# Kernel tuning notes

Hardware: AMD Instinct MI355X
Metric: run time of the kernel (lower is better)

Reference implementation:

```python
import jax, jax.numpy as jnp
import numpy as np

N = 50000
E = 800000
P = 400000
D_IN = 128
D_HID = 128


def setup_inputs() -> dict:
    key = jax.random.key(0)
    k = jax.random.split(key, 7)
    edge_index = jax.random.randint(k[0], (2, E), 0, N, dtype=jnp.int32)
    edge_pairs = jax.random.randint(k[1], (2, P), 0, N, dtype=jnp.int32)
    emb = jax.random.normal(k[2], (N, D_IN), dtype=jnp.float32)
    W1 = jax.random.normal(k[3], (D_IN, D_HID), dtype=jnp.float32) * (1.0 / np.sqrt(D_IN))
    b1 = jnp.zeros((D_HID,), dtype=jnp.float32)
    W2 = jax.random.normal(k[4], (D_HID, D_HID), dtype=jnp.float32) * (1.0 / np.sqrt(D_HID))
    b2 = jnp.zeros((D_HID,), dtype=jnp.float32)
    return {"edge_index": edge_index, "edge_pairs": edge_pairs, "emb": emb,
            "W1": W1, "b1": b1, "W2": W2, "b2": b2}


def gcn_conv(x, W, b, src, dst):
    """PyG GCNConv: add self-loops, symmetric deg^-1/2 normalization,
    linear transform, scatter-add aggregation into destination nodes."""
    n = x.shape[0]
    loop = jnp.arange(n, dtype=src.dtype)
    s = jnp.concatenate([src, loop])  # [E+N]
    d = jnp.concatenate([dst, loop])
    deg = jax.ops.segment_sum(jnp.ones_like(d, dtype=x.dtype), d, num_segments=n)
    dinv = jnp.where(deg > 0, jax.lax.rsqrt(jnp.maximum(deg, 1e-12)), 0.0)
    norm = dinv[s] * dinv[d]  # [E+N]
    h = x @ W  # [N, out]
    msg = h[s] * norm[:, None]  # gather + scale
    out = jax.ops.segment_sum(msg, d, num_segments=n)  # scatter-add
    return out + b


def reference(edge_index, edge_pairs, emb, W1, b1, W2, b2):
    src, dst = edge_index[0], edge_index[1]
    # encode (eval mode: dropout is identity)
    z = jax.nn.relu(gcn_conv(emb, W1, b1, src, dst))
    z = gcn_conv(z, W2, b2, src, dst)
    # decode: dot product per candidate pair
    return jnp.sum(z[edge_pairs[0]] * z[edge_pairs[1]], axis=1)  # [P]
```

## Files before the change

kernel.cpp:

```cpp
#include <hip/hip_runtime.h>


typedef __attribute__((ext_vector_type(8))) short short8;
typedef __attribute__((ext_vector_type(4))) float floatx4;

#define STAGE_G 128

__device__ __forceinline__ unsigned short f2bf(float f) {
    union { float f; unsigned int u; } v; v.f = f;
    unsigned int u = v.u;
    u += 0x7fffu + ((u >> 16) & 1u);
    return (unsigned short)(u >> 16);
}

__device__ __forceinline__ unsigned int pack2(float a, float b) {
    return (unsigned int)f2bf(a) | ((unsigned int)f2bf(b) << 16);
}

__device__ __forceinline__ float4 cvt4(uint2 u) {
    float4 f;
    f.x = __uint_as_float(u.x << 16);
    f.y = __uint_as_float(u.x & 0xffff0000u);
    f.z = __uint_as_float(u.y << 16);
    f.w = __uint_as_float(u.y & 0xffff0000u);
    return f;
}


__global__ __launch_bounds__(256) void block_hist_kernel(const int* __restrict__ dst,
                                                         int* __restrict__ bhist,
                                                         int E, int NB) {
    __shared__ int bh[1024];
    int t = threadIdx.x, g = blockIdx.x;
    for (int b = t; b < NB; b += 256) bh[b] = 0;
    __syncthreads();
    int chunk = (E + gridDim.x - 1) / gridDim.x;
    int lo = g * chunk, hi = min(lo + chunk, E);
    for (int i = lo + t; i < hi; i += 256) atomicAdd(&bh[dst[i] >> 6], 1);
    __syncthreads();
    for (int b = t; b < NB; b += 256) bhist[g * NB + b] = bh[b];
}

__global__ __launch_bounds__(128) void s1_scan_blocks(int* __restrict__ bhist,
                                                      int* __restrict__ T, int NB) {
    __shared__ int s[2][128];
    int b = blockIdx.x, t = threadIdx.x;
    int v = bhist[t * NB + b];
    int cur = 0;
    s[0][t] = v;
    __syncthreads();
#pragma unroll
    for (int off = 1; off < 128; off <<= 1) {
        int nxt = cur ^ 1;
        int val = s[cur][t];
        if (t >= off) val += s[cur][t - off];
        s[nxt][t] = val;
        __syncthreads();
        cur = nxt;
    }
    int inc = s[cur][t];
    bhist[t * NB + b] = inc - v;
    if (t == 127) T[b] = inc;
}

__global__ __launch_bounds__(256) void s2_scan_buckets(const int* __restrict__ T,
                                                       int* __restrict__ bucket_base, int NB) {
    __shared__ int sums[256];
    int t = threadIdx.x;
    int chunk = (NB + 255) >> 8;
    int lo = t * chunk, hi = min(lo + chunk, NB);
    int s = 0;
    for (int i = lo; i < hi; ++i) s += T[i];
    sums[t] = s;
    __syncthreads();
    if (t == 0) {
        int run = 0;
        for (int i = 0; i < 256; ++i) { int v = sums[i]; sums[i] = run; run += v; }
    }
    __syncthreads();
    int run = sums[t];
    for (int i = lo; i < hi; ++i) { bucket_base[i] = run; run += T[i]; }
    if (lo < NB && hi == NB) bucket_base[NB] = run;
}

__global__ __launch_bounds__(256) void stage_kernel(const int* __restrict__ src,
                                                    const int* __restrict__ dst,
                                                    const int* __restrict__ bhist,
                                                    const int* __restrict__ bucket_base,
                                                    unsigned int* __restrict__ stage,
                                                    int E, int NB) {
    __shared__ int lcur[1024];
    int t = threadIdx.x, g = blockIdx.x;
    for (int b = t; b < NB; b += 256) lcur[b] = bucket_base[b] + bhist[g * NB + b];
    __syncthreads();
    int chunk = (E + gridDim.x - 1) / gridDim.x;
    int lo = g * chunk, hi = min(lo + chunk, E);
    for (int i = lo + t; i < hi; i += 256) {
        int d = dst[i];
        int pos = atomicAdd(&lcur[d >> 6], 1);
        stage[pos] = ((unsigned int)src[i] << 6) | (unsigned int)(d & 63);
    }
}

__global__ __launch_bounds__(256) void scatter_kernel(const unsigned int* __restrict__ stage,
                                                      const int* __restrict__ bucket_base,
                                                      int* __restrict__ row_ptr,
                                                      float* __restrict__ dinv,
                                                      int* __restrict__ srcs_sorted,
                                                      int N) {
    __shared__ int cnt[64];
    __shared__ int lcur[64];
    int b = blockIdx.x, t = threadIdx.x;
    int lo = b << 6;
    int base = bucket_base[b], basen = bucket_base[b + 1];
    if (t < 64) cnt[t] = 0;
    __syncthreads();
    for (int i = base + t; i < basen; i += 256) atomicAdd(&cnt[stage[i] & 63u], 1);
    __syncthreads();
    if (t < 64) {
        int v = cnt[t];
        int inc = v;
#pragma unroll
        for (int off = 1; off < 64; off <<= 1) {
            int x = __shfl_up(inc, off, 64);
            if (t >= off) inc += x;
        }
        int exc = inc - v;
        int node = lo + t;
        if (node < N) {
            row_ptr[node] = base + exc;
            dinv[node] = rsqrtf((float)(v + 1));
            if (node == N - 1) row_ptr[N] = base + exc + v;
        }
        lcur[t] = base + exc;
    }
    __syncthreads();
    for (int i = base + t; i < basen; i += 256) {
        unsigned int rec = stage[i];
        int pos = atomicAdd(&lcur[rec & 63u], 1);
        srcs_sorted[pos] = (int)(rec >> 6);
    }
}

template <bool BF16IN>
__global__ __launch_bounds__(256) void gemm_mfma_kernel(const void* __restrict__ Xv,
                                                        const float* __restrict__ W,
                                                        const float* __restrict__ dinv,
                                                        uint2* __restrict__ H, int N) {
    __shared__ __align__(16) char smem[50176];
    short* WB = (short*)smem;
    short* XL = (short*)(smem + 32768);
    float* Cst = (float*)smem;

    const int tid = threadIdx.x;
    const int w = tid >> 6;
    const int lane = tid & 63;
    const int blk = blockIdx.x;

    {
        const float4* W4 = (const float4*)W;
#pragma unroll
        for (int i = 0; i < 16; ++i) {
            int f = tid + i * 256;
            int k = f >> 5;
            int c4 = f & 31;
            float4 wv = W4[f];
            int kt = k >> 5, q = (k >> 3) & 3, j = k & 7;
            float e[4] = {wv.x, wv.y, wv.z, wv.w};
#pragma unroll
            for (int m = 0; m < 4; ++m) {
                int c = c4 * 4 + m;
                int nt = c >> 4;
                int ln = q * 16 + (c & 15);
                WB[((nt * 4 + kt) * 64 + ln) * 8 + j] = (short)f2bf(e[m]);
            }
        }
    }
    {
#pragma unroll
        for (int i = 0; i < 8; ++i) {
            int f = tid + i * 256;
            int row = f >> 5;
            int c4 = f & 31;
            int gr = min(blk * 64 + row, N - 1);
            uint2 u;
            if constexpr (BF16IN) {
                u = ((const uint2*)Xv)[(size_t)gr * 32 + c4];
            } else {
                float4 xv = ((const float4*)Xv)[(size_t)gr * 32 + c4];
                u.x = pack2(xv.x, xv.y);
                u.y = pack2(xv.z, xv.w);
            }
            *(uint2*)&XL[row * 136 + c4 * 4] = u;
        }
    }
    __syncthreads();

    const int arow = w * 16 + (lane & 15);
    const int koff = (lane >> 4) * 8;
    short8 a[4];
#pragma unroll
    for (int kt = 0; kt < 4; ++kt)
        a[kt] = *(const short8*)&XL[arow * 136 + kt * 32 + koff];

    floatx4 acc[8];
#pragma unroll
    for (int nt = 0; nt < 8; ++nt) acc[nt] = (floatx4){0.f, 0.f, 0.f, 0.f};

#pragma unroll
    for (int kt = 0; kt < 4; ++kt) {
#pragma unroll
        for (int nt = 0; nt < 8; ++nt) {
            short8 b = *(const short8*)&WB[((nt * 4 + kt) * 64 + lane) * 8];
            acc[nt] = __builtin_amdgcn_mfma_f32_16x16x32_bf16(a[kt], b, acc[nt], 0, 0, 0);
        }
    }
    __syncthreads();

    {
        int q = lane >> 4, cn = lane & 15;
#pragma unroll
        for (int nt = 0; nt < 8; ++nt)
#pragma unroll
            for (int r = 0; r < 4; ++r)
                Cst[(w * 16 + q * 4 + r) * 132 + nt * 16 + cn] = acc[nt][r];
    }
    __syncthreads();
    {
#pragma unroll
        for (int i = 0; i < 8; ++i) {
            int f = tid + i * 256;
            int row = f >> 5;
            int c4 = f & 31;
            int gr = blk * 64 + row;
            if (gr < N) {
                float4 v = *(float4*)&Cst[row * 132 + c4 * 4];
                float di = dinv[gr];
                uint2 o;
                o.x = pack2(v.x * di, v.y * di);
                o.y = pack2(v.z * di, v.w * di);
                H[(size_t)gr * 32 + c4] = o;
            }
        }
    }
}

__global__ __launch_bounds__(256) void agg_kernel(const unsigned short* __restrict__ Hp,
                                                  const int* __restrict__ row_ptr,
                                                  const int* __restrict__ srcs,
                                                  const float* __restrict__ dinv,
                                                  const float* __restrict__ bias,
                                                  unsigned short* __restrict__ Z,
                                                  int N, int do_relu) {
    int gw = (int)((blockIdx.x * blockDim.x + threadIdx.x) >> 6);
    int lane = threadIdx.x & 63;
    int half = lane >> 5;
    int hl = lane & 31;
    int n = gw * 2 + half;
    if (n >= N) return;

    const uint2* H2 = (const uint2*)Hp;
    float4 a0 = cvt4(H2[(size_t)n * 32 + hl]);
    float4 a1 = make_float4(0.f, 0.f, 0.f, 0.f);
    float4 a2 = make_float4(0.f, 0.f, 0.f, 0.f);
    float4 a3 = make_float4(0.f, 0.f, 0.f, 0.f);

    int j = row_ptr[n], end = row_ptr[n + 1];
    for (; j + 7 < end; j += 8) {
        uint2 u0 = H2[(size_t)srcs[j + 0] * 32 + hl];
        uint2 u1 = H2[(size_t)srcs[j + 1] * 32 + hl];
        uint2 u2 = H2[(size_t)srcs[j + 2] * 32 + hl];
        uint2 u3 = H2[(size_t)srcs[j + 3] * 32 + hl];
        uint2 u4 = H2[(size_t)srcs[j + 4] * 32 + hl];
        uint2 u5 = H2[(size_t)srcs[j + 5] * 32 + hl];
        uint2 u6 = H2[(size_t)srcs[j + 6] * 32 + hl];
        uint2 u7 = H2[(size_t)srcs[j + 7] * 32 + hl];
        float4 t;
        t = cvt4(u0); a0.x += t.x; a0.y += t.y; a0.z += t.z; a0.w += t.w;
        t = cvt4(u1); a1.x += t.x; a1.y += t.y; a1.z += t.z; a1.w += t.w;
        t = cvt4(u2); a2.x += t.x; a2.y += t.y; a2.z += t.z; a2.w += t.w;
        t = cvt4(u3); a3.x += t.x; a3.y += t.y; a3.z += t.z; a3.w += t.w;
        t = cvt4(u4); a0.x += t.x; a0.y += t.y; a0.z += t.z; a0.w += t.w;
        t = cvt4(u5); a1.x += t.x; a1.y += t.y; a1.z += t.z; a1.w += t.w;
        t = cvt4(u6); a2.x += t.x; a2.y += t.y; a2.z += t.z; a2.w += t.w;
        t = cvt4(u7); a3.x += t.x; a3.y += t.y; a3.z += t.z; a3.w += t.w;
    }
    for (; j + 3 < end; j += 4) {
        uint2 u0 = H2[(size_t)srcs[j + 0] * 32 + hl];
        uint2 u1 = H2[(size_t)srcs[j + 1] * 32 + hl];
        uint2 u2 = H2[(size_t)srcs[j + 2] * 32 + hl];
        uint2 u3 = H2[(size_t)srcs[j + 3] * 32 + hl];
        float4 t;
        t = cvt4(u0); a0.x += t.x; a0.y += t.y; a0.z += t.z; a0.w += t.w;
        t = cvt4(u1); a1.x += t.x; a1.y += t.y; a1.z += t.z; a1.w += t.w;
        t = cvt4(u2); a2.x += t.x; a2.y += t.y; a2.z += t.z; a2.w += t.w;
        t = cvt4(u3); a3.x += t.x; a3.y += t.y; a3.z += t.z; a3.w += t.w;
    }
    for (; j < end; ++j) {
        float4 t = cvt4(H2[(size_t)srcs[j] * 32 + hl]);
        a0.x += t.x; a0.y += t.y; a0.z += t.z; a0.w += t.w;
    }
    a0.x += a1.x + a2.x + a3.x;
    a0.y += a1.y + a2.y + a3.y;
    a0.z += a1.z + a2.z + a3.z;
    a0.w += a1.w + a2.w + a3.w;

    float di = dinv[n];
    float4 bv = ((const float4*)bias)[hl];
    float ox = di * a0.x + bv.x;
    float oy = di * a0.y + bv.y;
    float oz = di * a0.z + bv.z;
    float ow = di * a0.w + bv.w;
    if (do_relu) {
        ox = fmaxf(ox, 0.f); oy = fmaxf(oy, 0.f);
        oz = fmaxf(oz, 0.f); ow = fmaxf(ow, 0.f);
    }
    uint2 o;
    o.x = pack2(ox, oy);
    o.y = pack2(oz, ow);
    ((uint2*)Z)[(size_t)n * 32 + hl] = o;
}

__global__ __launch_bounds__(256) void decode_kernel(const unsigned short* __restrict__ Z,
                                                     const int* __restrict__ pa,
                                                     const int* __restrict__ pb,
                                                     float* __restrict__ out, int P) {
    int grp = (int)((blockIdx.x * blockDim.x + threadIdx.x) >> 5);
    int hl = threadIdx.x & 31;
    int p0 = grp * 4;
    if (p0 >= P) return;
    const uint2* Z2 = (const uint2*)Z;

    if (p0 + 3 < P) {
        int A0 = pa[p0], A1 = pa[p0 + 1], A2 = pa[p0 + 2], A3 = pa[p0 + 3];
        int B0 = pb[p0], B1 = pb[p0 + 1], B2 = pb[p0 + 2], B3 = pb[p0 + 3];
        uint2 ua0 = Z2[(size_t)A0 * 32 + hl];
        uint2 ub0 = Z2[(size_t)B0 * 32 + hl];
        uint2 ua1 = Z2[(size_t)A1 * 32 + hl];
        uint2 ub1 = Z2[(size_t)B1 * 32 + hl];
        uint2 ua2 = Z2[(size_t)A2 * 32 + hl];
        uint2 ub2 = Z2[(size_t)B2 * 32 + hl];
        uint2 ua3 = Z2[(size_t)A3 * 32 + hl];
        uint2 ub3 = Z2[(size_t)B3 * 32 + hl];
        float4 va, vb;
        va = cvt4(ua0); vb = cvt4(ub0);
        float v0 = va.x * vb.x + va.y * vb.y + va.z * vb.z + va.w * vb.w;
        va = cvt4(ua1); vb = cvt4(ub1);
        float v1 = va.x * vb.x + va.y * vb.y + va.z * vb.z + va.w * vb.w;
        va = cvt4(ua2); vb = cvt4(ub2);
        float v2 = va.x * vb.x + va.y * vb.y + va.z * vb.z + va.w * vb.w;
        va = cvt4(ua3); vb = cvt4(ub3);
        float v3 = va.x * vb.x + va.y * vb.y + va.z * vb.z + va.w * vb.w;
#pragma unroll
        for (int off = 16; off > 0; off >>= 1) {
            v0 += __shfl_down(v0, off, 32);
            v1 += __shfl_down(v1, off, 32);
            v2 += __shfl_down(v2, off, 32);
            v3 += __shfl_down(v3, off, 32);
        }
        if (hl == 0) *(float4*)&out[p0] = make_float4(v0, v1, v2, v3);
    } else {
        for (int p = p0; p < P; ++p) {
            float4 va = cvt4(Z2[(size_t)pa[p] * 32 + hl]);
            float4 vb = cvt4(Z2[(size_t)pb[p] * 32 + hl]);
            float v = va.x * vb.x + va.y * vb.y + va.z * vb.z + va.w * vb.w;
#pragma unroll
            for (int off = 16; off > 0; off >>= 1) v += __shfl_down(v, off, 32);
            if (hl == 0) out[p] = v;
        }
    }
}

extern "C" void kernel_launch(void* const* d_in, const int* in_sizes, int n_in,
                              void* d_out, int out_size, void* d_ws, size_t ws_size,
                              hipStream_t stream) {
    const int*   edge_index = (const int*)d_in[0];
    const int*   edge_pairs = (const int*)d_in[1];
    const float* emb        = (const float*)d_in[2];
    const float* W1         = (const float*)d_in[3];
    const float* b1         = (const float*)d_in[4];
    const float* W2         = (const float*)d_in[5];
    const float* b2         = (const float*)d_in[6];
    float* out = (float*)d_out;

    int E = in_sizes[0] / 2;
    int P = in_sizes[1] / 2;
    int N = in_sizes[2] / 128;
    int NB = (N + 63) / 64;

    const int* src = edge_index;
    const int* dst = edge_index + E;
    const int* pa  = edge_pairs;
    const int* pb  = edge_pairs + P;

    char* ws = (char*)d_ws;
    size_t off = 0;
    auto alloc = [&](size_t bytes) -> void* {
        void* p = ws + off;
        off = (off + bytes + 255) & ~(size_t)255;
        return p;
    };
    unsigned short* bufA = (unsigned short*)alloc((size_t)N * 128 * 2);
    unsigned short* bufB = (unsigned short*)alloc((size_t)N * 128 * 2);
    int*   srcs_sorted  = (int*)alloc((size_t)E * sizeof(int));
    unsigned int* stage = (unsigned int*)alloc((size_t)E * sizeof(unsigned int));
    int*   row_ptr      = (int*)alloc((size_t)(N + 1) * sizeof(int));
    float* dinv         = (float*)alloc((size_t)N * sizeof(float));
    int*   bhist        = (int*)alloc((size_t)STAGE_G * NB * sizeof(int));
    int*   T            = (int*)alloc((size_t)NB * sizeof(int));
    int*   bucket_base  = (int*)alloc((size_t)(NB + 1) * sizeof(int));

    block_hist_kernel<<<STAGE_G, 256, 0, stream>>>(dst, bhist, E, NB);
    s1_scan_blocks<<<NB, 128, 0, stream>>>(bhist, T, NB);
    s2_scan_buckets<<<1, 256, 0, stream>>>(T, bucket_base, NB);
    stage_kernel<<<STAGE_G, 256, 0, stream>>>(src, dst, bhist, bucket_base, stage, E, NB);
    scatter_kernel<<<NB, 256, 0, stream>>>(stage, bucket_base, row_ptr, dinv, srcs_sorted, N);

    gemm_mfma_kernel<false><<<(N + 63) / 64, 256, 0, stream>>>(emb, W1, dinv, (uint2*)bufA, N);
    agg_kernel<<<(N + 7) / 8, 256, 0, stream>>>(bufA, row_ptr, srcs_sorted, dinv, b1, bufB, N, 1);

    gemm_mfma_kernel<true><<<(N + 63) / 64, 256, 0, stream>>>(bufB, W2, dinv, (uint2*)bufA, N);
    agg_kernel<<<(N + 7) / 8, 256, 0, stream>>>(bufA, row_ptr, srcs_sorted, dinv, b2, bufB, N, 0);

    decode_kernel<<<(P + 31) / 32, 256, 0, stream>>>(bufB, pa, pb, out, P);
}
```

Measured before the change: 248.3 us.

## Fuse CSR construction kernels into one cooperative kernel with grid syncs

Replaces the five CSR-building launches (histogram, two scans, staging, per-bucket scatter) with a single cooperative kernel that separates phases with grid.sync(). The histogram and staging phases now run on 512 blocks instead of 128, and the per-bucket scans and scatters loop over buckets with grid stride. This aims to remove launch gaps and raise parallelism in the edge passes. In exchange it adds grid-wide barrier costs, a larger block histogram to scan (512 rows per bucket), and fewer blocks for the bucket scatter phase.

Measured after the change: 492.3 us. +98.3%, slower.

```diff
diff --git a/kernel.cpp b/kernel.cpp
--- a/kernel.cpp
+++ b/kernel.cpp
@@ -1,10 +1,13 @@
 #include <hip/hip_runtime.h>
+#include <hip/hip_cooperative_groups.h>
+
+namespace cg = cooperative_groups;
 
 
 typedef __attribute__((ext_vector_type(8))) short short8;
 typedef __attribute__((ext_vector_type(4))) float floatx4;
 
-#define STAGE_G 128
+#define CSR_G 512
 
 __device__ __forceinline__ unsigned short f2bf(float f) {
     union { float f; unsigned int u; } v; v.f = f;
@@ -26,119 +29,116 @@
     return f;
 }
 
-
-__global__ __launch_bounds__(256) void block_hist_kernel(const int* __restrict__ dst,
-                                                         int* __restrict__ bhist,
-                                                         int E, int NB) {
-    __shared__ int bh[1024];
-    int t = threadIdx.x, g = blockIdx.x;
-    for (int b = t; b < NB; b += 256) bh[b] = 0;
-    __syncthreads();
-    int chunk = (E + gridDim.x - 1) / gridDim.x;
-    int lo = g * chunk, hi = min(lo + chunk, E);
-    for (int i = lo + t; i < hi; i += 256) atomicAdd(&bh[dst[i] >> 6], 1);
-    __syncthreads();
-    for (int b = t; b < NB; b += 256) bhist[g * NB + b] = bh[b];
-}
-
-__global__ __launch_bounds__(128) void s1_scan_blocks(int* __restrict__ bhist,
-                                                      int* __restrict__ T, int NB) {
-    __shared__ int s[2][128];
-    int b = blockIdx.x, t = threadIdx.x;
-    int v = bhist[t * NB + b];
-    int cur = 0;
-    s[0][t] = v;
-    __syncthreads();
-#pragma unroll
-    for (int off = 1; off < 128; off <<= 1) {
-        int nxt = cur ^ 1;
-        int val = s[cur][t];
-        if (t >= off) val += s[cur][t - off];
-        s[nxt][t] = val;
-        __syncthreads();
-        cur = nxt;
-    }
-    int inc = s[cur][t];
-    bhist[t * NB + b] = inc - v;
-    if (t == 127) T[b] = inc;
-}
-
-__global__ __launch_bounds__(256) void s2_scan_buckets(const int* __restrict__ T,
-                                                       int* __restrict__ bucket_base, int NB) {
-    __shared__ int sums[256];
-    int t = threadIdx.x;
-    int chunk = (NB + 255) >> 8;
-    int lo = t * chunk, hi = min(lo + chunk, NB);
-    int s = 0;
-    for (int i = lo; i < hi; ++i) s += T[i];
-    sums[t] = s;
-    __syncthreads();
-    if (t == 0) {
-        int run = 0;
-        for (int i = 0; i < 256; ++i) { int v = sums[i]; sums[i] = run; run += v; }
-    }
-    __syncthreads();
-    int run = sums[t];
-    for (int i = lo; i < hi; ++i) { bucket_base[i] = run; run += T[i]; }
-    if (lo < NB && hi == NB) bucket_base[NB] = run;
-}
-
-__global__ __launch_bounds__(256) void stage_kernel(const int* __restrict__ src,
-                                                    const int* __restrict__ dst,
-                                                    const int* __restrict__ bhist,
-                                                    const int* __restrict__ bucket_base,
-                                                    unsigned int* __restrict__ stage,
-                                                    int E, int NB) {
-    __shared__ int lcur[1024];
-    int t = threadIdx.x, g = blockIdx.x;
-    for (int b = t; b < NB; b += 256) lcur[b] = bucket_base[b] + bhist[g * NB + b];
-    __syncthreads();
-    int chunk = (E + gridDim.x - 1) / gridDim.x;
-    int lo = g * chunk, hi = min(lo + chunk, E);
-    for (int i = lo + t; i < hi; i += 256) {
+__global__ __launch_bounds__(256) void csr_coop_kernel(const int* __restrict__ src,
+                                                       const int* __restrict__ dst,
+                                                       int* __restrict__ bhist,
+                                                       int* __restrict__ T,
+                                                       int* __restrict__ bucket_base,
+                                                       unsigned int* __restrict__ stage,
+                                                       int* __restrict__ row_ptr,
+                                                       float* __restrict__ dinv,
+                                                       int* __restrict__ srcs_sorted,
+                                                       int E, int N, int NB) {
+    cg::grid_group grid = cg::this_grid();
+    __shared__ int sh[1024];
+    const int t = threadIdx.x, g = blockIdx.x;
+    const int G = CSR_G;
+    const int chunk = (E + G - 1) / G;
+    const int elo = g * chunk, ehi = min(elo + chunk, E);
+
+    for (int b = t; b < NB; b += 256) sh[b] = 0;
+    __syncthreads();
+    for (int i = elo + t; i < ehi; i += 256) atomicAdd(&sh[dst[i] >> 6], 1);
+    __syncthreads();
+    for (int b = t; b < NB; b += 256) bhist[(size_t)g * NB + b] = sh[b];
+
+    grid.sync();
+
+    for (int b = g; b < NB; b += G) {
+        int v0 = bhist[(size_t)(2 * t) * NB + b];
+        int v1 = bhist[(size_t)(2 * t + 1) * NB + b];
+        int s = v0 + v1;
+        int cur = 0;
+        sh[t] = s;
+        __syncthreads();
+#pragma unroll
+        for (int off = 1; off < 256; off <<= 1) {
+            int val = sh[cur * 256 + t];
+            if (t >= off) val += sh[cur * 256 + t - off];
+            sh[(1 - cur) * 256 + t] = val;
+            __syncthreads();
+            cur = 1 - cur;
+        }
+        int inc = sh[cur * 256 + t];
+        int exc = inc - s;
+        bhist[(size_t)(2 * t) * NB + b] = exc;
+        bhist[(size_t)(2 * t + 1) * NB + b] = exc + v0;
+        if (t == 255) T[b] = inc;
+        __syncthreads();
+    }
+
+    grid.sync();
+
+    if (g == 0) {
+        int cb = (NB + 255) >> 8;
+        int lo = t * cb, hi = min(lo + cb, NB);
+        int s = 0;
+        for (int i = lo; i < hi; ++i) s += T[i];
+        sh[t] = s;
+        __syncthreads();
+        if (t == 0) {
+            int run = 0;
+            for (int i = 0; i < 256; ++i) { int v = sh[i]; sh[i] = run; run += v; }
+        }
+        __syncthreads();
+        int run = sh[t];
+        for (int i = lo; i < hi; ++i) { bucket_base[i] = run; run += T[i]; }
+        if (lo < NB && hi == NB) bucket_base[NB] = run;
+    }
+
+    grid.sync();
+
+    for (int b = t; b < NB; b += 256) sh[b] = bucket_base[b] + bhist[(size_t)g * NB + b];
+    __syncthreads();
+    for (int i = elo + t; i < ehi; i += 256) {
         int d = dst[i];
-        int pos = atomicAdd(&lcur[d >> 6], 1);
+        int pos = atomicAdd(&sh[d >> 6], 1);
         stage[pos] = ((unsigned int)src[i] << 6) | (unsigned int)(d & 63);
     }
-}
-
-__global__ __launch_bounds__(256) void scatter_kernel(const unsigned int* __restrict__ stage,
-                                                      const int* __restrict__ bucket_base,
-                                                      int* __restrict__ row_ptr,
-                                                      float* __restrict__ dinv,
-                                                      int* __restrict__ srcs_sorted,
-                                                      int N) {
-    __shared__ int cnt[64];
-    __shared__ int lcur[64];
-    int b = blockIdx.x, t = threadIdx.x;
-    int lo = b << 6;
-    int base = bucket_base[b], basen = bucket_base[b + 1];
-    if (t < 64) cnt[t] = 0;
-    __syncthreads();
-    for (int i = base + t; i < basen; i += 256) atomicAdd(&cnt[stage[i] & 63u], 1);
-    __syncthreads();
-    if (t < 64) {
-        int v = cnt[t];
-        int inc = v;
-#pragma unroll
-        for (int off = 1; off < 64; off <<= 1) {
-            int x = __shfl_up(inc, off, 64);
-            if (t >= off) inc += x;
-        }
-        int exc = inc - v;
-        int node = lo + t;
-        if (node < N) {
-            row_ptr[node] = base + exc;
-            dinv[node] = rsqrtf((float)(v + 1));
-            if (node == N - 1) row_ptr[N] = base + exc + v;
-        }
-        lcur[t] = base + exc;
-    }
-    __syncthreads();
-    for (int i = base + t; i < basen; i += 256) {
-        unsigned int rec = stage[i];
-        int pos = atomicAdd(&lcur[rec & 63u], 1);
-        srcs_sorted[pos] = (int)(rec >> 6);
+
+    grid.sync();
+
+    for (int b = g; b < NB; b += G) {
+        int lob = b << 6;
+        int base = bucket_base[b], basen = bucket_base[b + 1];
+        if (t < 64) sh[t] = 0;
+        __syncthreads();
+        for (int i = base + t; i < basen; i += 256) atomicAdd(&sh[stage[i] & 63u], 1);
+        __syncthreads();
+        if (t < 64) {
+            int v = sh[t];
+            int inc = v;
+#pragma unroll
+            for (int off = 1; off < 64; off <<= 1) {
+                int x = __shfl_up(inc, off, 64);
+                if (t >= off) inc += x;
+            }
+            int exc = inc - v;
+            int node = lob + t;
+            if (node < N) {
+                row_ptr[node] = base + exc;
+                dinv[node] = rsqrtf((float)(v + 1));
+                if (node == N - 1) row_ptr[N] = base + exc + v;
+            }
+            sh[64 + t] = base + exc;
+        }
+        __syncthreads();
+        for (int i = base + t; i < basen; i += 256) {
+            unsigned int rec = stage[i];
+            int pos = atomicAdd(&sh[64 + (rec & 63u)], 1);
+            srcs_sorted[pos] = (int)(rec >> 6);
+        }
+        __syncthreads();
     }
 }
 
@@ -406,15 +406,18 @@
     unsigned int* stage = (unsigned int*)alloc((size_t)E * sizeof(unsigned int));
     int*   row_ptr      = (int*)alloc((size_t)(N + 1) * sizeof(int));
     float* dinv         = (float*)alloc((size_t)N * sizeof(float));
-    int*   bhist        = (int*)alloc((size_t)STAGE_G * NB * sizeof(int));
+    int*   bhist        = (int*)alloc((size_t)CSR_G * NB * sizeof(int));
     int*   T            = (int*)alloc((size_t)NB * sizeof(int));
     int*   bucket_base  = (int*)alloc((size_t)(NB + 1) * sizeof(int));
 
-    block_hist_kernel<<<STAGE_G, 256, 0, stream>>>(dst, bhist, E, NB);
-    s1_scan_blocks<<<NB, 128, 0, stream>>>(bhist, T, NB);
-    s2_scan_buckets<<<1, 256, 0, stream>>>(T, bucket_base, NB);
-    stage_kernel<<<STAGE_G, 256, 0, stream>>>(src, dst, bhist, bucket_base, stage, E, NB);
-    scatter_kernel<<<NB, 256, 0, stream>>>(stage, bucket_base, row_ptr, dinv, srcs_sorted, N);
+    {
+        void* args[] = {(void*)&src, (void*)&dst, (void*)&bhist, (void*)&T,
+                        (void*)&bucket_base, (void*)&stage, (void*)&row_ptr,
+                        (void*)&dinv, (void*)&srcs_sorted,
+                        (void*)&E, (void*)&N, (void*)&NB};
+        hipLaunchCooperativeKernel((void*)csr_coop_kernel, dim3(CSR_G), dim3(256),
+                                   args, 0, stream);
+    }
 
     gemm_mfma_kernel<false><<<(N + 63) / 64, 256, 0, stream>>>(emb, W1, dinv, (uint2*)bufA, N);
     agg_kernel<<<(N + 7) / 8, 256, 0, stream>>>(bufA, row_ptr, srcs_sorted, dinv, b1, bufB, N, 1);
```
